# Performance work log

Measured on AMD Instinct MI355X. Metric: run time of the kernel, lower is better.

## Reference

```python
import jax, jax.numpy as jnp
import numpy as np

H = 128  # hidden size
I = 6    # input size after concat

def setup_inputs() -> dict:
    key = jax.random.key(0)
    ks = jax.random.split(key, 12)
    B, T = 2048, 168
    s_inp = jax.random.normal(ks[0], (B, T, 5), dtype=jnp.float32)
    flow_x = jax.random.normal(ks[1], (B, T, 1), dtype=jnp.float32)
    sc = 1.0 / np.sqrt(H)
    # PyTorch LSTM params: gate order i, f, g, o
    W_ih = jax.random.uniform(ks[2], (4 * H, I), jnp.float32, -sc, sc)
    W_hh = jax.random.uniform(ks[3], (4 * H, H), jnp.float32, -sc, sc)
    b_ih = jax.random.uniform(ks[4], (4 * H,), jnp.float32, -sc, sc)
    b_hh = jax.random.uniform(ks[5], (4 * H,), jnp.float32, -sc, sc)
    sc1 = 1.0 / np.sqrt(128)
    W1 = jax.random.uniform(ks[6], (64, 128), jnp.float32, -sc1, sc1)
    b1 = jax.random.uniform(ks[7], (64,), jnp.float32, -sc1, sc1)
    a1 = jnp.array(0.25, dtype=jnp.float32)  # PReLU weight
    sc2 = 1.0 / np.sqrt(64)
    W2 = jax.random.uniform(ks[8], (1, 64), jnp.float32, -sc2, sc2)
    b2 = jax.random.uniform(ks[9], (1,), jnp.float32, -sc2, sc2)
    a2 = jnp.array(0.25, dtype=jnp.float32)
    return {"s_inp": s_inp, "flow_x": flow_x, "W_ih": W_ih, "W_hh": W_hh,
            "b_ih": b_ih, "b_hh": b_hh, "W1": W1, "b1": b1, "a1": a1,
            "W2": W2, "b2": b2, "a2": a2}

def _prelu(x, a):
    return jnp.where(x >= 0, x, a * x)

def _lstm_last(x, W_ih, W_hh, b_ih, b_hh):
    # x: [B, T, I] -> last hidden state h_T: [B, H]
    B = x.shape[0]
    # precompute input contribution for all timesteps: [T, B, 4H]
    x_gates = jnp.einsum('bti,gi->tbg', x, W_ih) + (b_ih + b_hh)

    def step(carry, xg):
        h, c = carry
        gates = xg + h @ W_hh.T  # [B, 4H]
        i, f, g, o = jnp.split(gates, 4, axis=-1)
        i = jax.nn.sigmoid(i)
        f = jax.nn.sigmoid(f)
        g = jnp.tanh(g)
        o = jax.nn.sigmoid(o)
        c = f * c + i * g
        h = o * jnp.tanh(c)
        return (h, c), None

    h0 = jnp.zeros((B, H), dtype=x.dtype)
    c0 = jnp.zeros((B, H), dtype=x.dtype)
    (h, c), _ = jax.lax.scan(step, (h0, c0), x_gates)
    return h

def reference(s_inp, flow_x, W_ih, W_hh, b_ih, b_hh, W1, b1, a1, W2, b2, a2):
    x = jnp.concatenate([s_inp, flow_x], axis=2)  # [B, T, 6]
    h_last = _lstm_last(x, W_ih, W_hh, b_ih, b_hh)  # [B, 128]
    y = _prelu(h_last @ W1.T + b1, a1)              # [B, 64]
    y = _prelu(y @ W2.T + b2, a2)                   # [B, 1]
    return y
```

## Files before the change

### kernel.cpp

```cpp
#include <hip/hip_runtime.h>


typedef __attribute__((ext_vector_type(8))) short short8;
typedef __attribute__((ext_vector_type(4))) float f32x4;

#define BT 512
#define TS 168
#define HID 128
#define AROW 320
#define ABUF (8 * AROW)
#define NNT 4

__device__ __forceinline__ ushort bf_hi(float v) {
    return (ushort)(__float_as_uint(v) >> 16);
}
__device__ __forceinline__ ushort bf_lo(float v) {
    unsigned h = __float_as_uint(v) & 0xFFFF0000u;
    float l = v - __uint_as_float(h);
    return (ushort)(__float_as_uint(l) >> 16);
}
__device__ __forceinline__ float sigm_f(float x) {
    return __fdividef(1.f, 1.f + __expf(-x));
}
__device__ __forceinline__ float tanh_f(float x) {
    return 1.f - __fdividef(2.f, __expf(2.f * x) + 1.f);
}

__global__ __launch_bounds__(BT, 2) void lstm_mfma8_kernel(
    const float* __restrict__ s_inp,
    const float* __restrict__ flow_x,
    const float* __restrict__ W_ih,
    const float* __restrict__ W_hh,
    const float* __restrict__ b_ih,
    const float* __restrict__ b_hh,
    const float* __restrict__ W1,
    const float* __restrict__ b1,
    const float* __restrict__ a1p,
    const float* __restrict__ W2,
    const float* __restrict__ b2,
    const float* __restrict__ a2p,
    float* __restrict__ out)
{
    __shared__ float xs[8][TS][6];
    __shared__ __align__(16) ushort hA[2 * ABUF];
    __shared__ float y1s[8][64];

    const int t = threadIdx.x;
    const int w = t >> 6;
    const int l = t & 63;
    const int l15 = l & 15;
    const int l4 = l >> 4;
    const int row_base = blockIdx.x * 8;

    short8 P1s[5][NNT], P2s[5][NNT];
    #pragma unroll
    for (int nt = 0; nt < NNT; ++nt) {
        const int gc = nt * HID + w * 16 + l15;
        const float bias = b_ih[gc] + b_hh[gc];
        #pragma unroll
        for (int q = 0; q < 4; ++q) {
            #pragma unroll
            for (int j = 0; j < 8; ++j) {
                float v = W_hh[gc * HID + q * 32 + l4 * 8 + j];
                P1s[q][nt][j] = (short)bf_hi(v);
                P2s[q][nt][j] = (short)bf_lo(v);
            }
        }
        #pragma unroll
        for (int j = 0; j < 8; ++j) {
            int u = l4 * 8 + j;
            float v = (u < 6)  ? W_ih[gc * 6 + u]
                    : (u < 12) ? W_ih[gc * 6 + (u - 6)]
                    : (u == 12) ? bias : 0.f;
            P1s[4][nt][j] = (short)bf_hi(v);
            P2s[4][nt][j] = (short)bf_lo(v);
        }
    }

    for (int idx = t; idx < 8 * TS * 5; idx += BT) {
        int r = idx / (TS * 5), rem = idx % (TS * 5);
        xs[r][rem / 5][rem % 5] = s_inp[(size_t)row_base * (TS * 5) + idx];
    }
    for (int idx = t; idx < 8 * TS; idx += BT) {
        xs[idx / TS][idx % TS][5] = flow_x[(size_t)row_base * TS + idx];
    }
    for (int idx = t; idx < 2 * ABUF / 2; idx += BT)
        ((unsigned*)hA)[idx] = 0u;
    __syncthreads();

    if (t < 16) {
        int b = t >> 3, r = t & 7;
        int byte = (2 * 268) ^ (r << 4);
        hA[b * ABUF + r * AROW + (byte >> 1)] = 0x3F80;
    }
    const bool xhi = (t < 48);
    const bool xlo = (t >= 64 && t < 112);
    const int xu = xhi ? t : (t - 64);
    const int xr = (xu < 48) ? (xu / 6) : 0;
    const int xi = (xu < 48) ? (xu % 6) : 0;
    const int xslot = xhi ? (256 + xi) : (262 + xi);
    const int xw_idx = xr * AROW + ((((2 * xslot) ^ ((xr & 7) << 4))) >> 1);
    if (xhi | xlo) {
        float v = xs[xr][0][xi];
        hA[xw_idx] = xhi ? bf_hi(v) : bf_lo(v);
    }

    const int arow = l15 & 7;
    const int a_base = arow * AROW;
    const int a_swz = arow << 4;
    const int ch = w * 16 + l15;
    const bool lowhalf = (l < 32);
    const int rbase = (l4 & 1) * 4 + (lowhalf ? 0 : 2);
    const int row0 = rbase, row1 = rbase + 1;
    const int hw0 = row0 * AROW + ((((2 * ch) ^ (row0 << 4))) >> 1);
    const int hw1 = row1 * AROW + ((((2 * ch) ^ (row1 << 4))) >> 1);

    float c0 = 0.f, c1 = 0.f, h0f = 0.f, h1f = 0.f;
    int rb = 0, wbo = ABUF;

    for (int s = 0; s < TS; ++s) {
        __syncthreads();

        f32x4 acc[NNT];
        #pragma unroll
        for (int nt = 0; nt < NNT; ++nt) acc[nt] = (f32x4){0.f, 0.f, 0.f, 0.f};

        #pragma unroll
        for (int kk = 0; kk < 9; ++kk) {
            const int q = (kk < 4) ? kk : ((kk < 8) ? kk - 4 : 4);
            int off = ((kk * 64 + l4 * 16) ^ a_swz) >> 1;
            short8 a = *(const short8*)(hA + rb + a_base + off);
            #pragma unroll
            for (int nt = 0; nt < NNT; ++nt)
                acc[nt] = __builtin_amdgcn_mfma_f32_16x16x32_bf16(a, P1s[q][nt], acc[nt], 0, 0, 0);
            if (kk < 4 || kk == 8) {
                #pragma unroll
                for (int nt = 0; nt < NNT; ++nt)
                    acc[nt] = __builtin_amdgcn_mfma_f32_16x16x32_bf16(a, P2s[q][nt], acc[nt], 0, 0, 0);
            }
        }

        if ((xhi | xlo) && s + 1 < TS) {
            float v = xs[xr][s + 1][xi];
            hA[wbo + xw_idx] = xhi ? bf_hi(v) : bf_lo(v);
        }

        float gi0 = lowhalf ? acc[0][0] : acc[0][2];
        float gf0 = lowhalf ? acc[1][0] : acc[1][2];
        float gg0 = lowhalf ? acc[2][0] : acc[2][2];
        float go0 = lowhalf ? acc[3][0] : acc[3][2];
        float gi1 = lowhalf ? acc[0][1] : acc[0][3];
        float gf1 = lowhalf ? acc[1][1] : acc[1][3];
        float gg1 = lowhalf ? acc[2][1] : acc[2][3];
        float go1 = lowhalf ? acc[3][1] : acc[3][3];

        {
            float ia = sigm_f(gi0);
            float fa = sigm_f(gf0);
            float ga = tanh_f(gg0);
            float oa = sigm_f(go0);
            c0 = fa * c0 + ia * ga;
            h0f = oa * tanh_f(c0);
            hA[wbo + hw0] = bf_hi(h0f);
            hA[wbo + hw0 + 128] = bf_lo(h0f);
        }
        {
            float ia = sigm_f(gi1);
            float fa = sigm_f(gf1);
            float ga = tanh_f(gg1);
            float oa = sigm_f(go1);
            c1 = fa * c1 + ia * ga;
            h1f = oa * tanh_f(c1);
            hA[wbo + hw1] = bf_hi(h1f);
            hA[wbo + hw1 + 128] = bf_lo(h1f);
        }

        int tmp = rb; rb = wbo; wbo = tmp;
    }
    __syncthreads();

    float* hfin = (float*)xs;
    hfin[row0 * HID + ch] = h0f;
    hfin[row1 * HID + ch] = h1f;
    __syncthreads();

    {
        int r = t >> 6, j = t & 63;
        const float4* wrow = (const float4*)(W1 + j * HID);
        const float4* hr = (const float4*)(hfin + r * HID);
        float acc = b1[j];
        #pragma unroll
        for (int q = 0; q < HID / 4; ++q) {
            float4 a = hr[q], b = wrow[q];
            acc += a.x * b.x + a.y * b.y + a.z * b.z + a.w * b.w;
        }
        float av = a1p[0];
        y1s[r][j] = (acc >= 0.f) ? acc : av * acc;
    }
    __syncthreads();

    if (t < 8) {
        const float4* w2 = (const float4*)W2;
        const float4* yr = (const float4*)&y1s[t][0];
        float acc = 0.f;
        #pragma unroll
        for (int q = 0; q < 64 / 4; ++q) {
            float4 a = yr[q], b = w2[q];
            acc += a.x * b.x + a.y * b.y + a.z * b.z + a.w * b.w;
        }
        acc += b2[0];
        float av = a2p[0];
        out[row_base + t] = (acc >= 0.f) ? acc : av * acc;
    }
}

extern "C" void kernel_launch(void* const* d_in, const int* in_sizes, int n_in,
                              void* d_out, int out_size, void* d_ws, size_t ws_size,
                              hipStream_t stream) {
    const float* s_inp  = (const float*)d_in[0];
    const float* flow_x = (const float*)d_in[1];
    const float* W_ih   = (const float*)d_in[2];
    const float* W_hh   = (const float*)d_in[3];
    const float* b_ih   = (const float*)d_in[4];
    const float* b_hh   = (const float*)d_in[5];
    const float* W1     = (const float*)d_in[6];
    const float* b1     = (const float*)d_in[7];
    const float* a1     = (const float*)d_in[8];
    const float* W2     = (const float*)d_in[9];
    const float* b2     = (const float*)d_in[10];
    const float* a2     = (const float*)d_in[11];
    float* out = (float*)d_out;

    dim3 grid(2048 / 8);
    dim3 block(BT);
    lstm_mfma8_kernel<<<grid, block, 0, stream>>>(
        s_inp, flow_x, W_ih, W_hh, b_ih, b_hh, W1, b1, a1, W2, b2, a2, out);
}
```

Measured before the change: 268.2 us.

## Split gate columns across 16 waves with swapped MFMA operands

Doubles the block to 1024 threads (16 waves), each handling 8 hidden channels with two MFMA tiles instead of four. MFMA operands are swapped so the weights are the A operand and the hidden state is B, and weight rows are interleaved so one accumulator holds the i,f,g,o gates of one channel. This removes the lane-select shuffling and halves the serial MFMA chain per wave on each recurrent step. In exchange, half the lanes compute duplicate outputs that are masked on write, and the larger block may raise the cost of each per-step barrier.

After: 334.7 us. 24.8% more time.

```diff
diff --git a/kernel.cpp b/kernel.cpp
--- a/kernel.cpp
+++ b/kernel.cpp
@@ -4,12 +4,12 @@
 typedef __attribute__((ext_vector_type(8))) short short8;
 typedef __attribute__((ext_vector_type(4))) float f32x4;
 
-#define BT 512
+#define BT 1024
 #define TS 168
 #define HID 128
 #define AROW 320
 #define ABUF (8 * AROW)
-#define NNT 4
+#define NNT 2
 
 __device__ __forceinline__ ushort bf_hi(float v) {
     return (ushort)(__float_as_uint(v) >> 16);
@@ -26,7 +26,7 @@
     return 1.f - __fdividef(2.f, __expf(2.f * x) + 1.f);
 }
 
-__global__ __launch_bounds__(BT, 2) void lstm_mfma8_kernel(
+__global__ __launch_bounds__(BT, 4) void lstm_mfma10_kernel(
     const float* __restrict__ s_inp,
     const float* __restrict__ flow_x,
     const float* __restrict__ W_ih,
@@ -55,13 +55,13 @@
     short8 P1s[5][NNT], P2s[5][NNT];
     #pragma unroll
     for (int nt = 0; nt < NNT; ++nt) {
-        const int gc = nt * HID + w * 16 + l15;
-        const float bias = b_ih[gc] + b_hh[gc];
+        const int wrow = (l15 & 3) * HID + w * 8 + nt * 4 + (l15 >> 2);
+        const float bias = b_ih[wrow] + b_hh[wrow];
         #pragma unroll
         for (int q = 0; q < 4; ++q) {
             #pragma unroll
             for (int j = 0; j < 8; ++j) {
-                float v = W_hh[gc * HID + q * 32 + l4 * 8 + j];
+                float v = W_hh[wrow * HID + q * 32 + l4 * 8 + j];
                 P1s[q][nt][j] = (short)bf_hi(v);
                 P2s[q][nt][j] = (short)bf_lo(v);
             }
@@ -69,8 +69,8 @@
         #pragma unroll
         for (int j = 0; j < 8; ++j) {
             int u = l4 * 8 + j;
-            float v = (u < 6)  ? W_ih[gc * 6 + u]
-                    : (u < 12) ? W_ih[gc * 6 + (u - 6)]
+            float v = (u < 6)  ? W_ih[wrow * 6 + u]
+                    : (u < 12) ? W_ih[wrow * 6 + (u - 6)]
                     : (u == 12) ? bias : 0.f;
             P1s[4][nt][j] = (short)bf_hi(v);
             P2s[4][nt][j] = (short)bf_lo(v);
@@ -84,7 +84,7 @@
     for (int idx = t; idx < 8 * TS; idx += BT) {
         xs[idx / TS][idx % TS][5] = flow_x[(size_t)row_base * TS + idx];
     }
-    for (int idx = t; idx < 2 * ABUF / 2; idx += BT)
+    for (int idx = t; idx < ABUF; idx += BT)
         ((unsigned*)hA)[idx] = 0u;
     __syncthreads();
 
@@ -108,12 +108,11 @@
     const int arow = l15 & 7;
     const int a_base = arow * AROW;
     const int a_swz = arow << 4;
-    const int ch = w * 16 + l15;
-    const bool lowhalf = (l < 32);
-    const int rbase = (l4 & 1) * 4 + (lowhalf ? 0 : 2);
-    const int row0 = rbase, row1 = rbase + 1;
-    const int hw0 = row0 * AROW + ((((2 * ch) ^ (row0 << 4))) >> 1);
-    const int hw1 = row1 * AROW + ((((2 * ch) ^ (row1 << 4))) >> 1);
+    const int ch0 = w * 8 + l4;
+    const int ch1 = w * 8 + 4 + l4;
+    const bool wr_en = (l15 < 8);
+    const int hw0 = arow * AROW + ((((2 * ch0) ^ (arow << 4))) >> 1);
+    const int hw1 = arow * AROW + ((((2 * ch1) ^ (arow << 4))) >> 1);
 
     float c0 = 0.f, c1 = 0.f, h0f = 0.f, h1f = 0.f;
     int rb = 0, wbo = ABUF;
@@ -121,22 +120,19 @@
     for (int s = 0; s < TS; ++s) {
         __syncthreads();
 
-        f32x4 acc[NNT];
-        #pragma unroll
-        for (int nt = 0; nt < NNT; ++nt) acc[nt] = (f32x4){0.f, 0.f, 0.f, 0.f};
+        f32x4 acc0 = (f32x4){0.f, 0.f, 0.f, 0.f};
+        f32x4 acc1 = (f32x4){0.f, 0.f, 0.f, 0.f};
 
         #pragma unroll
         for (int kk = 0; kk < 9; ++kk) {
             const int q = (kk < 4) ? kk : ((kk < 8) ? kk - 4 : 4);
             int off = ((kk * 64 + l4 * 16) ^ a_swz) >> 1;
-            short8 a = *(const short8*)(hA + rb + a_base + off);
-            #pragma unroll
-            for (int nt = 0; nt < NNT; ++nt)
-                acc[nt] = __builtin_amdgcn_mfma_f32_16x16x32_bf16(a, P1s[q][nt], acc[nt], 0, 0, 0);
+            short8 b = *(const short8*)(hA + rb + a_base + off);
+            acc0 = __builtin_amdgcn_mfma_f32_16x16x32_bf16(P1s[q][0], b, acc0, 0, 0, 0);
+            acc1 = __builtin_amdgcn_mfma_f32_16x16x32_bf16(P1s[q][1], b, acc1, 0, 0, 0);
             if (kk < 4 || kk == 8) {
-                #pragma unroll
-                for (int nt = 0; nt < NNT; ++nt)
-                    acc[nt] = __builtin_amdgcn_mfma_f32_16x16x32_bf16(a, P2s[q][nt], acc[nt], 0, 0, 0);
+                acc0 = __builtin_amdgcn_mfma_f32_16x16x32_bf16(P2s[q][0], b, acc0, 0, 0, 0);
+                acc1 = __builtin_amdgcn_mfma_f32_16x16x32_bf16(P2s[q][1], b, acc1, 0, 0, 0);
             }
         }
 
@@ -145,34 +141,29 @@
             hA[wbo + xw_idx] = xhi ? bf_hi(v) : bf_lo(v);
         }
 
-        float gi0 = lowhalf ? acc[0][0] : acc[0][2];
-        float gf0 = lowhalf ? acc[1][0] : acc[1][2];
-        float gg0 = lowhalf ? acc[2][0] : acc[2][2];
-        float go0 = lowhalf ? acc[3][0] : acc[3][2];
-        float gi1 = lowhalf ? acc[0][1] : acc[0][3];
-        float gf1 = lowhalf ? acc[1][1] : acc[1][3];
-        float gg1 = lowhalf ? acc[2][1] : acc[2][3];
-        float go1 = lowhalf ? acc[3][1] : acc[3][3];
-
         {
-            float ia = sigm_f(gi0);
-            float fa = sigm_f(gf0);
-            float ga = tanh_f(gg0);
-            float oa = sigm_f(go0);
+            float ia = sigm_f(acc0[0]);
+            float fa = sigm_f(acc0[1]);
+            float ga = tanh_f(acc0[2]);
+            float oa = sigm_f(acc0[3]);
             c0 = fa * c0 + ia * ga;
             h0f = oa * tanh_f(c0);
-            hA[wbo + hw0] = bf_hi(h0f);
-            hA[wbo + hw0 + 128] = bf_lo(h0f);
+            if (wr_en) {
+                hA[wbo + hw0] = bf_hi(h0f);
+                hA[wbo + hw0 + 128] = bf_lo(h0f);
+            }
         }
         {
-            float ia = sigm_f(gi1);
-            float fa = sigm_f(gf1);
-            float ga = tanh_f(gg1);
-            float oa = sigm_f(go1);
+            float ia = sigm_f(acc1[0]);
+            float fa = sigm_f(acc1[1]);
+            float ga = tanh_f(acc1[2]);
+            float oa = sigm_f(acc1[3]);
             c1 = fa * c1 + ia * ga;
             h1f = oa * tanh_f(c1);
-            hA[wbo + hw1] = bf_hi(h1f);
-            hA[wbo + hw1 + 128] = bf_lo(h1f);
+            if (wr_en) {
+                hA[wbo + hw1] = bf_hi(h1f);
+                hA[wbo + hw1 + 128] = bf_lo(h1f);
+            }
         }
 
         int tmp = rb; rb = wbo; wbo = tmp;
@@ -180,11 +171,13 @@
     __syncthreads();
 
     float* hfin = (float*)xs;
-    hfin[row0 * HID + ch] = h0f;
-    hfin[row1 * HID + ch] = h1f;
-    __syncthreads();
-
-    {
+    if (wr_en) {
+        hfin[arow * HID + ch0] = h0f;
+        hfin[arow * HID + ch1] = h1f;
+    }
+    __syncthreads();
+
+    if (t < 512) {
         int r = t >> 6, j = t & 63;
         const float4* wrow = (const float4*)(W1 + j * HID);
         const float4* hr = (const float4*)(hfin + r * HID);
@@ -233,6 +226,6 @@
 
     dim3 grid(2048 / 8);
     dim3 block(BT);
-    lstm_mfma8_kernel<<<grid, block, 0, stream>>>(
+    lstm_mfma10_kernel<<<grid, block, 0, stream>>>(
         s_inp, flow_x, W_ih, W_hh, b_ih, b_hh, W1, b1, a1, W2, b2, a2, out);
 }
```
